# Optimization experiments

Measured on AMD Instinct MI355X. Metric: run time of the kernel, lower is better.

## Reference

```python
import math
import jax, jax.numpy as jnp
import numpy as np

NUM_HEADS, RAD_PTS, LVL_PTS = 8, 4, 1
P = RAD_PTS * LVL_PTS


def setup_inputs() -> dict:
    B, Nq, Din = 2, 21760, 256
    hw = np.array([[128, 128], [64, 64], [32, 32], [16, 16]], np.int64)
    sizes = hw[:, 0] * hw[:, 1]
    offs = np.concatenate([[0], np.cumsum(sizes)[:-1]]).astype(np.int64)
    Ns = int(sizes.sum())
    map_ids = np.tile(np.repeat(np.arange(4), sizes)[None], (B, 1)).astype(np.int64)

    key = jax.random.key(0)
    ks = jax.random.split(key, 8)
    in_feats = jax.random.normal(ks[0], (B, Nq, Din), jnp.float32)
    sample_feats = jax.random.normal(ks[1], (B, Ns, Din), jnp.float32)
    sample_priors = jax.random.uniform(ks[2], (B, Nq, 2), jnp.float32)

    # sample_offsets bias: radial grid init as in the torch module
    thetas = np.arange(NUM_HEADS) * (2.0 * math.pi / NUM_HEADS)
    grid = np.stack([np.cos(thetas), np.sin(thetas), np.zeros(NUM_HEADS)], 1)
    grid = grid / np.abs(grid).max(1, keepdims=True)
    grid = np.tile(grid.reshape(NUM_HEADS, 1, 1, 3), (1, RAD_PTS, LVL_PTS, 1))
    grid = grid * np.arange(1, RAD_PTS + 1).reshape(1, RAD_PTS, 1, 1)
    bo = jnp.asarray(grid.reshape(-1), jnp.float32)

    Wo = jax.random.normal(ks[3], (NUM_HEADS * P * 3, Din), jnp.float32) * 0.01
    Wa = jax.random.normal(ks[4], (NUM_HEADS * P, Din), jnp.float32) * 0.01
    ba = jnp.zeros((NUM_HEADS * P,), jnp.float32)
    s = 1.0 / np.sqrt(Din)
    Wv = jax.random.normal(ks[5], (Din, Din), jnp.float32) * s
    bv = jnp.zeros((Din,), jnp.float32)
    Wout = jax.random.normal(ks[6], (Din, Din), jnp.float32) * s
    bout = jnp.zeros((Din,), jnp.float32)

    return dict(in_feats=in_feats, sample_priors=sample_priors, sample_feats=sample_feats,
                map_hw=jnp.asarray(hw), map_offs=jnp.asarray(offs), map_ids=jnp.asarray(map_ids),
                Wo=Wo, bo=bo, Wa=Wa, ba=ba, Wv=Wv, bv=bv, Wout=Wout, bout=bout)


def _trilinear_sample(val, map_hw, map_offs, xy, z, L):
    # val [B,Ns,H,D]; xy [B,Q,H,P,2] normalized; z [B,Q,H,P] in ~[0,1]
    B, Ns, H, D = val.shape
    Q = xy.shape[1]
    val_t = val.transpose(0, 2, 1, 3)  # [B,H,Ns,D]
    x, y = xy[..., 0], xy[..., 1]
    lvl_f = z * (L - 1)
    l0 = jnp.floor(lvl_f).astype(jnp.int32)
    wz = lvl_f - l0.astype(lvl_f.dtype)

    def gather(idx):  # idx [B,Q,H,P] int32 -> [B,Q,H,P,D]
        it = idx.transpose(0, 2, 1, 3).reshape(B, H, Q * P, 1)
        g = jnp.take_along_axis(val_t, it, axis=2)  # [B,H,Q*P,D]
        return g.reshape(B, H, Q, P, D).transpose(0, 2, 1, 3, 4)

    def sample_level(lvl):  # bilinear sample within pyramid level `lvl` (zero padding)
        valid_l = (lvl >= 0) & (lvl < L)
        lc = jnp.clip(lvl, 0, L - 1)
        Hl = map_hw[lc, 0].astype(jnp.int32)
        Wl = map_hw[lc, 1].astype(jnp.int32)
        off = map_offs[lc].astype(jnp.int32)
        xf = x * Wl.astype(x.dtype) - 0.5
        yf = y * Hl.astype(x.dtype) - 0.5
        x0 = jnp.floor(xf).astype(jnp.int32)
        y0 = jnp.floor(yf).astype(jnp.int32)
        dx = xf - x0.astype(x.dtype)
        dy = yf - y0.astype(x.dtype)
        out = jnp.zeros((B, Q, H, P, D), x.dtype)
        corners = [(x0, y0, (1 - dx) * (1 - dy)), (x0 + 1, y0, dx * (1 - dy)),
                   (x0, y0 + 1, (1 - dx) * dy), (x0 + 1, y0 + 1, dx * dy)]
        for xi, yi, w in corners:
            ok = valid_l & (xi >= 0) & (xi < Wl) & (yi >= 0) & (yi < Hl)
            idx = off + jnp.clip(yi, 0, Hl - 1) * Wl + jnp.clip(xi, 0, Wl - 1)
            out = out + gather(idx) * (w * ok.astype(x.dtype))[..., None]
        return out

    return sample_level(l0) * (1 - wz)[..., None] + sample_level(l0 + 1) * wz[..., None]


def reference(in_feats, sample_priors, sample_feats, map_hw, map_offs, map_ids,
              Wo, bo, Wa, ba, Wv, bv, Wout, bout):
    B, Nq, _ = in_feats.shape
    Ns = sample_feats.shape[1]
    L = map_hw.shape[0]
    D = Wv.shape[0] // NUM_HEADS

    val = (sample_feats @ Wv.T + bv).reshape(B, Ns, NUM_HEADS, D)
    offs = (in_feats @ Wo.T + bo).reshape(B, Nq, NUM_HEADS, P, 3)

    # sample_priors last dim == 2: normalize offsets by (W, H) of the query's map
    norm = map_hw[:, ::-1][map_ids].astype(offs.dtype)  # [B,Nq,2] (w,h)
    sample_xy = sample_priors[:, :, None, None, :2] + offs[..., :2] / norm[:, :, None, None, :]

    lvl_off = jnp.arange(LVL_PTS, dtype=offs.dtype) - 0.5 * (LVL_PTS - 1)
    z_grid = map_ids[:, :, None, None, None].astype(offs.dtype) + lvl_off  # [B,Nq,1,1,Lp]
    z_grid = jnp.broadcast_to(z_grid, (B, Nq, NUM_HEADS, RAD_PTS, LVL_PTS)).reshape(B, Nq, NUM_HEADS, P)
    sample_z = (z_grid + jnp.tanh(offs[..., 2])) / (L - 1)

    attn = jax.nn.softmax((in_feats @ Wa.T + ba).reshape(B, Nq, NUM_HEADS, P), axis=3)

    sampled = _trilinear_sample(val, map_hw, map_offs, sample_xy, sample_z, L)  # [B,Nq,H,P,D]
    attn_feats = jnp.einsum('bqhpd,bqhp->bqhd', sampled, attn).reshape(B, Nq, NUM_HEADS * D)
    return attn_feats @ Wout.T + bout
```

## Files before the change

### kernel.cpp

```cpp
#include <hip/hip_runtime.h>
#include <hip/hip_bf16.h>
#include <math.h>

typedef __bf16 bf16x8 __attribute__((ext_vector_type(8)));
typedef float f32x4 __attribute__((ext_vector_type(4)));
typedef float f32x2 __attribute__((ext_vector_type(2)));
typedef unsigned short ushort8 __attribute__((ext_vector_type(8)));

static __device__ __forceinline__ unsigned short f2bf(float f) {
    union { float f; unsigned u; } c; c.f = f;
    unsigned r = c.u + 0x7FFFu + ((c.u >> 16) & 1u);
    return (unsigned short)(r >> 16);
}

__global__ __launch_bounds__(256) void convert_weights_hist(
    const float* __restrict__ Wv, const float* __restrict__ Wo,
    const float* __restrict__ Wa, const float* __restrict__ Wout,
    const float* __restrict__ bo, const float* __restrict__ ba,
    unsigned short* __restrict__ Wv_b, unsigned short* __restrict__ Woa_b,
    unsigned short* __restrict__ Wout_b, float* __restrict__ boa,
    const float* __restrict__ priors, int* __restrict__ counts,
    int BQ, int Nq)
{
    __shared__ int cnt[16];
    if (threadIdx.x < 16) cnt[threadIdx.x] = 0;
    __syncthreads();

    int gid = blockIdx.x * blockDim.x + threadIdx.x;
    int stride = gridDim.x * blockDim.x;
    for (int i = gid; i < 163840; i += stride) {
        if (i < 65536)       Wv_b[i] = f2bf(Wv[i]);
        else if (i < 90112)  Woa_b[i - 65536] = f2bf(Wo[i - 65536]);
        else if (i < 98304)  Woa_b[i - 65536] = f2bf(Wa[i - 90112]);
        else                 Wout_b[i - 98304] = f2bf(Wout[i - 98304]);
    }
    if (gid < 96)       boa[gid] = bo[gid];
    else if (gid < 128) boa[gid] = ba[gid - 96];

    for (int q = gid; q < BQ; q += stride) {
        int b = q / Nq;
        float py = priors[(size_t)q * 2 + 1];
        int band = min(7, max(0, (int)(py * 8.0f)));
        atomicAdd(&cnt[b * 8 + band], 1);
    }
    __syncthreads();
    if (threadIdx.x < 16 && cnt[threadIdx.x] > 0)
        atomicAdd(&counts[threadIdx.x], cnt[threadIdx.x]);
}

__global__ __launch_bounds__(256) void bucket_scatter(
    const float* __restrict__ priors, const int* __restrict__ counts,
    int* __restrict__ cursors, int* __restrict__ qidx, int BQ, int Nq)
{
    __shared__ int lcnt[16];
    __shared__ int lbase[16];
    const int tid = threadIdx.x;
    if (tid < 16) lcnt[tid] = 0;
    __syncthreads();
    int q = blockIdx.x * 256 + tid;
    int mybucket = 0, myslot = 0;
    bool valid = q < BQ;
    if (valid) {
        int b = q / Nq;
        float py = priors[(size_t)q * 2 + 1];
        int band = min(7, max(0, (int)(py * 8.0f)));
        mybucket = b * 8 + band;
        myslot = atomicAdd(&lcnt[mybucket], 1);
    }
    __syncthreads();
    if (tid < 16) {
        int base = 0;
        #pragma unroll
        for (int i = 0; i < 16; ++i) base += (i < tid) ? counts[i] : 0;
        lbase[tid] = base + atomicAdd(&cursors[tid], lcnt[tid]);
    }
    __syncthreads();
    if (valid) qidx[lbase[mybucket] + myslot] = q;
}

template<int WN, bool A_BF16, int OUT_MODE>
__global__ __launch_bounds__(WN * 64) void gemm_mfma(
    const void* __restrict__ Av, const unsigned short* __restrict__ W,
    const float* __restrict__ bias, void* __restrict__ Cv,
    int M, int N, int K, int NsPB)
{
    constexpr int BM = 64;
    constexpr int BN = WN * 64;
    constexpr int BK = 64;
    constexpr int NTHR = WN * 64;
    constexpr int LDP = 72;

    __shared__ __align__(16) unsigned short smem[(BM + BN) * LDP];
    unsigned short* As = smem;
    unsigned short* Bs = smem + BM * LDP;

    const int bm  = blockIdx.x * BM;
    const int bn  = blockIdx.y * BN;
    const int tid = threadIdx.x;
    const int wid = tid >> 6;
    const int lane = tid & 63;
    const int lr = lane & 15;
    const int lg = lane >> 4;

    f32x4 acc[4][4];
    #pragma unroll
    for (int mi = 0; mi < 4; ++mi)
        #pragma unroll
        for (int ni = 0; ni < 4; ++ni)
            acc[mi][ni] = (f32x4){0.f, 0.f, 0.f, 0.f};

    for (int kt = 0; kt < K; kt += BK) {
        if (A_BF16) {
            const unsigned short* A = (const unsigned short*)Av;
            #pragma unroll
            for (int u = tid; u < BM * 8; u += NTHR) {
                int r = u >> 3, kb = u & 7;
                ushort8 v = *(const ushort8*)(A + (size_t)(bm + r) * K + kt + kb * 8);
                *(ushort8*)(As + r * LDP + kb * 8) = v;
            }
        } else {
            const float* A = (const float*)Av;
            #pragma unroll
            for (int u = tid; u < BM * 8; u += NTHR) {
                int r = u >> 3, kb = u & 7;
                const float* src = A + (size_t)(bm + r) * K + kt + kb * 8;
                float4 f0 = *(const float4*)(src);
                float4 f1 = *(const float4*)(src + 4);
                ushort8 v;
                v[0] = f2bf(f0.x); v[1] = f2bf(f0.y);
                v[2] = f2bf(f0.z); v[3] = f2bf(f0.w);
                v[4] = f2bf(f1.x); v[5] = f2bf(f1.y);
                v[6] = f2bf(f1.z); v[7] = f2bf(f1.w);
                *(ushort8*)(As + r * LDP + kb * 8) = v;
            }
        }
        #pragma unroll
        for (int u = tid; u < BN * 8; u += NTHR) {
            int r = u >> 3, kb = u & 7;
            ushort8 v = *(const ushort8*)(W + (size_t)(bn + r) * K + kt + kb * 8);
            *(ushort8*)(Bs + r * LDP + kb * 8) = v;
        }
        __syncthreads();

        #pragma unroll
        for (int kk = 0; kk < 2; ++kk) {
            bf16x8 fa[4], fb[4];
            #pragma unroll
            for (int mi = 0; mi < 4; ++mi)
                fa[mi] = *(const bf16x8*)(As + (mi * 16 + lr) * LDP + kk * 32 + lg * 8);
            #pragma unroll
            for (int ni = 0; ni < 4; ++ni)
                fb[ni] = *(const bf16x8*)(Bs + (wid * 64 + ni * 16 + lr) * LDP + kk * 32 + lg * 8);
            #pragma unroll
            for (int mi = 0; mi < 4; ++mi)
                #pragma unroll
                for (int ni = 0; ni < 4; ++ni)
                    acc[mi][ni] = __builtin_amdgcn_mfma_f32_16x16x32_bf16(
                        fa[mi], fb[ni], acc[mi][ni], 0, 0, 0);
        }
        __syncthreads();
    }

    if (OUT_MODE == 2) {
        const int b = bm / NsPB;
        const int ns_base = bm - b * NsPB;
        #pragma unroll
        for (int ni = 0; ni < 4; ++ni) {
            int col = wid * 64 + ni * 16 + lr;
            int h   = col >> 5;
            int ch  = col & 31;
            float bv = bias[col];
            unsigned short* dst = (unsigned short*)Cv +
                (size_t)(b * 8 + h) * NsPB * 32 + ch;
            #pragma unroll
            for (int mi = 0; mi < 4; ++mi) {
                #pragma unroll
                for (int r = 0; r < 4; ++r) {
                    int ns = ns_base + mi * 16 + lg * 4 + r;
                    dst[(size_t)ns * 32] = f2bf(acc[mi][ni][r] + bv);
                }
            }
        }
    } else {
        #pragma unroll
        for (int ni = 0; ni < 4; ++ni) {
            int col = bn + wid * 64 + ni * 16 + lr;
            float bv = bias[col];
            #pragma unroll
            for (int mi = 0; mi < 4; ++mi) {
                #pragma unroll
                for (int r = 0; r < 4; ++r) {
                    int row = bm + mi * 16 + lg * 4 + r;
                    if (OUT_MODE == 1) {
                        ((unsigned short*)Cv)[(size_t)row * N + col] =
                            f2bf(acc[mi][ni][r] + bv);
                    } else {
                        ((float*)Cv)[(size_t)row * N + col] = acc[mi][ni][r] + bv;
                    }
                }
            }
        }
    }
}

__global__ __launch_bounds__(256) void msda_sample_kernel(
    const float* __restrict__ C1,
    const float* __restrict__ priors,
    const unsigned short* __restrict__ val,
    const int*   __restrict__ map_hw,
    const int*   __restrict__ map_offs,
    const int*   __restrict__ map_ids,
    const int*   __restrict__ qidx,
    unsigned short* __restrict__ out,
    int Nq, int Ns)
{
    const int swz = (blockIdx.x & 7) * (gridDim.x >> 3) + (blockIdx.x >> 3);
    const int qh  = threadIdx.x >> 7;
    const int bq  = qidx[swz * 2 + qh];
    const int t   = threadIdx.x & 127;
    const int b   = bq / Nq;
    const int q   = bq - b * Nq;

    __shared__ float s_w[2][32][9];
    __shared__ int   s_i[2][32][9];
    __shared__ float s_red[2][32][9];

    if (t < 32) {
        const int h = t >> 2;
        const int p = t & 3;
        const float* sc = C1 + (size_t)bq * 128;
        float o0 = sc[h * 12 + p * 3 + 0];
        float o1 = sc[h * 12 + p * 3 + 1];
        float o2 = sc[h * 12 + p * 3 + 2];
        float logit = sc[96 + h * 4 + p];

        float m = logit;
        m = fmaxf(m, __shfl_xor(m, 1));
        m = fmaxf(m, __shfl_xor(m, 2));
        float e = expf(logit - m);
        float s = e;
        s += __shfl_xor(s, 1);
        s += __shfl_xor(s, 2);
        float attnw = e / s;

        int lid = map_ids[(size_t)b * Ns + q];
        float px = priors[(size_t)bq * 2 + 0];
        float py = priors[(size_t)bq * 2 + 1];
        int Hq = map_hw[lid * 2 + 0];
        int Wq = map_hw[lid * 2 + 1];
        float x = px + o0 / (float)Wq;
        float y = py + o1 / (float)Hq;

        float lvl_f = (float)lid + tanhf(o2);
        float l0f = floorf(lvl_f);
        int   l0  = (int)l0f;
        float wz  = lvl_f - l0f;

        #pragma unroll
        for (int sl = 0; sl < 2; ++sl) {
            int   lv = l0 + sl;
            float wl = sl ? wz : (1.0f - wz);
            float w4[4];
            int   i4[4];
            if (lv >= 0 && lv < 4) {
                int Hs  = map_hw[lv * 2 + 0];
                int Ws  = map_hw[lv * 2 + 1];
                int off = map_offs[lv];
                float xf = x * (float)Ws - 0.5f;
                float yf = y * (float)Hs - 0.5f;
                float x0f = floorf(xf), y0f = floorf(yf);
                int   x0  = (int)x0f,  y0  = (int)y0f;
                float dx = xf - x0f, dy = yf - y0f;
                #pragma unroll
                for (int j = 0; j < 4; ++j) {
                    int xi = x0 + (j & 1);
                    int yi = y0 + (j >> 1);
                    float w = ((j & 1) ? dx : 1.0f - dx) *
                              ((j >> 1) ? dy : 1.0f - dy);
                    bool ok = (xi >= 0) && (xi < Ws) && (yi >= 0) && (yi < Hs);
                    w4[j] = ok ? (w * wl * attnw) : 0.0f;
                    i4[j] = ok ? ((off + yi * Ws + xi) << 6) : 0;
                }
            } else {
                #pragma unroll
                for (int j = 0; j < 4; ++j) { w4[j] = 0.0f; i4[j] = 0; }
            }
            #pragma unroll
            for (int j = 0; j < 4; ++j) {
                s_w[qh][t][sl * 4 + j] = w4[j];
                s_i[qh][t][sl * 4 + j] = i4[j];
            }
        }
    }
    __syncthreads();

    const int p  = t >> 5;
    const int s  = t & 31;
    const int h  = s >> 2;
    const int d8 = s & 3;
    const int hp = h * 4 + p;

    float w[8];
    int   ix[8];
    #pragma unroll
    for (int j = 0; j < 8; ++j) { w[j] = s_w[qh][hp][j]; ix[j] = s_i[qh][hp][j]; }

    const char* vbase = (const char*)(val + (size_t)(b * 8 + h) * Ns * 32) + d8 * 16;
    f32x2 acc2[4];
    #pragma unroll
    for (int k = 0; k < 4; ++k) acc2[k] = (f32x2){0.f, 0.f};

    #pragma unroll
    for (int j = 0; j < 8; ++j) {
        uint4 u = *(const uint4*)(vbase + ix[j]);
        f32x2 w2 = {w[j], w[j]};
        unsigned ua[4] = {u.x, u.y, u.z, u.w};
        #pragma unroll
        for (int k = 0; k < 4; ++k) {
            union { unsigned u; float f; } lo, hi;
            lo.u = ua[k] << 16;
            hi.u = ua[k] & 0xffff0000u;
            f32x2 v2 = {lo.f, hi.f};
            acc2[k] += w2 * v2;
        }
    }

    #pragma unroll
    for (int k = 0; k < 4; ++k) {
        acc2[k][0] += __shfl_xor(acc2[k][0], 32);
        acc2[k][1] += __shfl_xor(acc2[k][1], 32);
    }

    if (t >= 64 && t < 96) {
        #pragma unroll
        for (int k = 0; k < 4; ++k) {
            s_red[qh][t - 64][2 * k]     = acc2[k][0];
            s_red[qh][t - 64][2 * k + 1] = acc2[k][1];
        }
    }
    __syncthreads();

    if (t < 32) {
        ushort8 o;
        #pragma unroll
        for (int k = 0; k < 4; ++k) {
            o[2 * k]     = f2bf(acc2[k][0] + s_red[qh][t][2 * k]);
            o[2 * k + 1] = f2bf(acc2[k][1] + s_red[qh][t][2 * k + 1]);
        }
        *(ushort8*)(out + (size_t)bq * 256 + t * 8) = o;
    }
}

extern "C" void kernel_launch(void* const* d_in, const int* in_sizes, int n_in,
                              void* d_out, int out_size, void* d_ws, size_t ws_size,
                              hipStream_t stream) {
    const float* in_feats      = (const float*)d_in[0];
    const float* sample_priors = (const float*)d_in[1];
    const float* sample_feats  = (const float*)d_in[2];
    const int*   map_hw        = (const int*)d_in[3];
    const int*   map_offs      = (const int*)d_in[4];
    const int*   map_ids       = (const int*)d_in[5];
    const float* Wo            = (const float*)d_in[6];
    const float* bo            = (const float*)d_in[7];
    const float* Wa            = (const float*)d_in[8];
    const float* ba            = (const float*)d_in[9];
    const float* Wv            = (const float*)d_in[10];
    const float* bv            = (const float*)d_in[11];
    const float* Wout          = (const float*)d_in[12];
    const float* bout          = (const float*)d_in[13];
    float* out = (float*)d_out;

    const int B = 2, Nq = 21760, Din = 256;
    const int Ns = in_sizes[2] / (B * Din);
    const int BQ = B * Nq;

    unsigned short* val = (unsigned short*)d_out;
    float* C1 = (float*)d_ws;
    unsigned short* af = (unsigned short*)((char*)d_ws + (size_t)BQ * 128 * 4);
    char* wbase = (char*)d_ws + (size_t)BQ * 128 * 4 + (size_t)BQ * 256 * 2;
    unsigned short* Wv_b   = (unsigned short*)wbase;
    unsigned short* Woa_b  = Wv_b + 65536;
    unsigned short* Wout_b = Woa_b + 32768;
    float* boa = (float*)(Wout_b + 65536);
    int* bws  = (int*)(boa + 128);
    int* qidx = bws + 32;

    hipMemsetAsync(bws, 0, 128, stream);

    convert_weights_hist<<<dim3(160), dim3(256), 0, stream>>>(
        Wv, Wo, Wa, Wout, bo, ba, Wv_b, Woa_b, Wout_b, boa,
        sample_priors, bws, BQ, Nq);

    bucket_scatter<<<dim3((BQ + 255) / 256), dim3(256), 0, stream>>>(
        sample_priors, bws, bws + 16, qidx, BQ, Nq);

    gemm_mfma<4, false, 2><<<dim3(BQ / 64, 1), dim3(256), 0, stream>>>(
        sample_feats, Wv_b, bv, val, B * Ns, 256, Din, Ns);

    gemm_mfma<2, false, 0><<<dim3(BQ / 64, 1), dim3(128), 0, stream>>>(
        in_feats, Woa_b, boa, C1, BQ, 128, Din, Ns);

    msda_sample_kernel<<<dim3(BQ / 2), dim3(256), 0, stream>>>(
        C1, sample_priors, val, map_hw, map_offs, map_ids, qidx, af, Nq, Ns);

    gemm_mfma<4, true, 0><<<dim3(BQ / 64, 1), dim3(256), 0, stream>>>(
        af, Wout_b, bout, out, BQ, 256, Din, Ns);
}
```

Before: 130.9 us.

## Load GEMM tiles via direct global-to-LDS with XOR swizzle; split sample setup across 64 threads

The bf16 GEMM tiles (weights, and activations when already bf16) now go straight from global memory into LDS with the global_load_lds builtin, stored in an XOR-swizzled 64-wide layout in place of the padded row layout. Fragment reads apply the same swizzle to avoid bank conflicts. This skips the register round-trip on tile loads. Separately, the deformable-sampling setup spreads the two level slices over 64 threads instead of looping in 32, with the softmax shuffle distances adjusted to match. The swizzled layout and the lane-to-row mapping must agree exactly, or the MFMA inputs will be wrong.

New measurement: 114.2 us. 1.15x faster.

```diff
diff --git a/kernel.cpp b/kernel.cpp
--- a/kernel.cpp
+++ b/kernel.cpp
@@ -11,6 +11,14 @@
     union { float f; unsigned u; } c; c.f = f;
     unsigned r = c.u + 0x7FFFu + ((c.u >> 16) & 1u);
     return (unsigned short)(r >> 16);
+}
+
+static __device__ __forceinline__ void gload_lds16(
+    const unsigned short* g, unsigned short* l)
+{
+    __builtin_amdgcn_global_load_lds(
+        (const __attribute__((address_space(1))) void*)g,
+        (__attribute__((address_space(3))) void*)l, 16, 0, 0);
 }
 
 __global__ __launch_bounds__(256) void convert_weights_hist(
@@ -89,10 +97,10 @@
     constexpr int BK = 64;
     constexpr int NTHR = WN * 64;
     constexpr int LDP = 72;
-
-    __shared__ __align__(16) unsigned short smem[(BM + BN) * LDP];
-    unsigned short* As = smem;
-    unsigned short* Bs = smem + BM * LDP;
+    constexpr int ASZ = A_BF16 ? (BM * 64) : (BM * LDP);
+
+    __shared__ __align__(16) unsigned short As[ASZ];
+    __shared__ __align__(16) unsigned short Bs[BN * 64];
 
     const int bm  = blockIdx.x * BM;
     const int bn  = blockIdx.y * BN;
@@ -101,6 +109,8 @@
     const int lane = tid & 63;
     const int lr = lane & 15;
     const int lg = lane >> 4;
+    const int lrow = lane >> 3;
+    const int lc16 = (lane & 7) ^ (lrow & 7);
 
     f32x4 acc[4][4];
     #pragma unroll
@@ -110,13 +120,19 @@
             acc[mi][ni] = (f32x4){0.f, 0.f, 0.f, 0.f};
 
     for (int kt = 0; kt < K; kt += BK) {
+        #pragma unroll
+        for (int c = wid; c < BN / 8; c += WN) {
+            const unsigned short* g =
+                W + (size_t)(bn + c * 8 + lrow) * K + kt + lc16 * 8;
+            gload_lds16(g, Bs + c * 512);
+        }
         if (A_BF16) {
             const unsigned short* A = (const unsigned short*)Av;
             #pragma unroll
-            for (int u = tid; u < BM * 8; u += NTHR) {
-                int r = u >> 3, kb = u & 7;
-                ushort8 v = *(const ushort8*)(A + (size_t)(bm + r) * K + kt + kb * 8);
-                *(ushort8*)(As + r * LDP + kb * 8) = v;
+            for (int c = wid; c < BM / 8; c += WN) {
+                const unsigned short* g =
+                    A + (size_t)(bm + c * 8 + lrow) * K + kt + lc16 * 8;
+                gload_lds16(g, As + c * 512);
             }
         } else {
             const float* A = (const float*)Av;
@@ -134,23 +150,28 @@
                 *(ushort8*)(As + r * LDP + kb * 8) = v;
             }
         }
-        #pragma unroll
-        for (int u = tid; u < BN * 8; u += NTHR) {
-            int r = u >> 3, kb = u & 7;
-            ushort8 v = *(const ushort8*)(W + (size_t)(bn + r) * K + kt + kb * 8);
-            *(ushort8*)(Bs + r * LDP + kb * 8) = v;
-        }
         __syncthreads();
 
         #pragma unroll
         for (int kk = 0; kk < 2; ++kk) {
             bf16x8 fa[4], fb[4];
             #pragma unroll
-            for (int mi = 0; mi < 4; ++mi)
-                fa[mi] = *(const bf16x8*)(As + (mi * 16 + lr) * LDP + kk * 32 + lg * 8);
-            #pragma unroll
-            for (int ni = 0; ni < 4; ++ni)
-                fb[ni] = *(const bf16x8*)(Bs + (wid * 64 + ni * 16 + lr) * LDP + kk * 32 + lg * 8);
+            for (int mi = 0; mi < 4; ++mi) {
+                if (A_BF16) {
+                    int row = mi * 16 + lr;
+                    fa[mi] = *(const bf16x8*)(As + row * 64 +
+                                              ((kk * 4 + lg) ^ (lr & 7)) * 8);
+                } else {
+                    fa[mi] = *(const bf16x8*)(As + (mi * 16 + lr) * LDP +
+                                              kk * 32 + lg * 8);
+                }
+            }
+            #pragma unroll
+            for (int ni = 0; ni < 4; ++ni) {
+                int row = wid * 64 + ni * 16 + lr;
+                fb[ni] = *(const bf16x8*)(Bs + row * 64 +
+                                          ((kk * 4 + lg) ^ (lr & 7)) * 8);
+            }
             #pragma unroll
             for (int mi = 0; mi < 4; ++mi)
                 #pragma unroll
@@ -225,22 +246,22 @@
     __shared__ int   s_i[2][32][9];
     __shared__ float s_red[2][32][9];
 
-    if (t < 32) {
-        const int h = t >> 2;
-        const int p = t & 3;
+    if (t < 64) {
+        const int hp = t >> 1;
+        const int sl = t & 1;
         const float* sc = C1 + (size_t)bq * 128;
-        float o0 = sc[h * 12 + p * 3 + 0];
-        float o1 = sc[h * 12 + p * 3 + 1];
-        float o2 = sc[h * 12 + p * 3 + 2];
-        float logit = sc[96 + h * 4 + p];
+        float o0 = sc[hp * 3 + 0];
+        float o1 = sc[hp * 3 + 1];
+        float o2 = sc[hp * 3 + 2];
+        float logit = sc[96 + hp];
 
         float m = logit;
-        m = fmaxf(m, __shfl_xor(m, 1));
         m = fmaxf(m, __shfl_xor(m, 2));
+        m = fmaxf(m, __shfl_xor(m, 4));
         float e = expf(logit - m);
         float s = e;
-        s += __shfl_xor(s, 1);
         s += __shfl_xor(s, 2);
+        s += __shfl_xor(s, 4);
         float attnw = e / s;
 
         int lid = map_ids[(size_t)b * Ns + q];
@@ -256,40 +277,37 @@
         int   l0  = (int)l0f;
         float wz  = lvl_f - l0f;
 
-        #pragma unroll
-        for (int sl = 0; sl < 2; ++sl) {
-            int   lv = l0 + sl;
-            float wl = sl ? wz : (1.0f - wz);
-            float w4[4];
-            int   i4[4];
-            if (lv >= 0 && lv < 4) {
-                int Hs  = map_hw[lv * 2 + 0];
-                int Ws  = map_hw[lv * 2 + 1];
-                int off = map_offs[lv];
-                float xf = x * (float)Ws - 0.5f;
-                float yf = y * (float)Hs - 0.5f;
-                float x0f = floorf(xf), y0f = floorf(yf);
-                int   x0  = (int)x0f,  y0  = (int)y0f;
-                float dx = xf - x0f, dy = yf - y0f;
-                #pragma unroll
-                for (int j = 0; j < 4; ++j) {
-                    int xi = x0 + (j & 1);
-                    int yi = y0 + (j >> 1);
-                    float w = ((j & 1) ? dx : 1.0f - dx) *
-                              ((j >> 1) ? dy : 1.0f - dy);
-                    bool ok = (xi >= 0) && (xi < Ws) && (yi >= 0) && (yi < Hs);
-                    w4[j] = ok ? (w * wl * attnw) : 0.0f;
-                    i4[j] = ok ? ((off + yi * Ws + xi) << 6) : 0;
-                }
-            } else {
-                #pragma unroll
-                for (int j = 0; j < 4; ++j) { w4[j] = 0.0f; i4[j] = 0; }
-            }
+        const int   lv = l0 + sl;
+        const float wl = sl ? wz : (1.0f - wz);
+        float w4[4];
+        int   i4[4];
+        if (lv >= 0 && lv < 4) {
+            int Hs  = map_hw[lv * 2 + 0];
+            int Ws  = map_hw[lv * 2 + 1];
+            int off = map_offs[lv];
+            float xf = x * (float)Ws - 0.5f;
+            float yf = y * (float)Hs - 0.5f;
+            float x0f = floorf(xf), y0f = floorf(yf);
+            int   x0  = (int)x0f,  y0  = (int)y0f;
+            float dx = xf - x0f, dy = yf - y0f;
             #pragma unroll
             for (int j = 0; j < 4; ++j) {
-                s_w[qh][t][sl * 4 + j] = w4[j];
-                s_i[qh][t][sl * 4 + j] = i4[j];
-            }
+                int xi = x0 + (j & 1);
+                int yi = y0 + (j >> 1);
+                float w = ((j & 1) ? dx : 1.0f - dx) *
+                          ((j >> 1) ? dy : 1.0f - dy);
+                bool ok = (xi >= 0) && (xi < Ws) && (yi >= 0) && (yi < Hs);
+                w4[j] = ok ? (w * wl * attnw) : 0.0f;
+                i4[j] = ok ? ((off + yi * Ws + xi) << 6) : 0;
+            }
+        } else {
+            #pragma unroll
+            for (int j = 0; j < 4; ++j) { w4[j] = 0.0f; i4[j] = 0; }
+        }
+        #pragma unroll
+        for (int j = 0; j < 4; ++j) {
+            s_w[qh][hp][sl * 4 + j] = w4[j];
+            s_i[qh][hp][sl * 4 + j] = i4[j];
         }
     }
     __syncthreads();
```
